# Kernel optimization log

Hardware: AMD Instinct MI355X
Metric: run time of the kernel (lower is better)

## Reference

```python
import jax, jax.numpy as jnp
import numpy as np

N = 100000
E = 1600000
D = 128


def setup_inputs() -> dict:
    key = jax.random.key(0)
    ks = jax.random.split(key, 6)
    x = jax.random.normal(ks[0], (N, D), dtype=jnp.float32)
    edge_row = jax.random.randint(ks[1], (E,), 0, N)
    edge_col = jax.random.randint(ks[2], (E,), 0, N)
    edge_val = jax.random.uniform(ks[3], (E,), dtype=jnp.float32)
    # Kaiming-ish init for the MLP weights
    W1 = jax.random.normal(ks[4], (D, D), dtype=jnp.float32) * (1.0 / np.sqrt(D))
    W2 = jax.random.normal(ks[5], (D, D), dtype=jnp.float32) * (1.0 / np.sqrt(D))
    b1 = jnp.zeros((D,), dtype=jnp.float32)
    b2 = jnp.zeros((D,), dtype=jnp.float32)
    eps = jnp.zeros((1,), dtype=jnp.float32)  # GIN eps, init 0
    bias = jnp.zeros((D,), dtype=jnp.float32)
    return {"x": x, "edge_row": edge_row, "edge_col": edge_col, "edge_val": edge_val,
            "W1": W1, "b1": b1, "W2": W2, "b2": b2, "eps": eps, "bias": bias}


def reference(x, edge_row, edge_col, edge_val, W1, b1, W2, b2, eps, bias):
    # sparse adj @ x : out[i] = sum_{edges (i,j)} val * x[j]
    agg = jax.ops.segment_sum(edge_val[:, None] * x[edge_col], edge_row, num_segments=N)
    h = (1.0 + eps) * x + agg                     # eps-scaled residual, [N, D]
    h = jax.nn.relu(h @ W1 + b1)                  # MLP layer 1
    h = jax.nn.relu(h @ W2 + b2)                  # MLP layer 2
    out = jax.nn.relu(h + bias)                   # bias + final relu
    return out
```

## Files before the change

### kernel.cpp

```cpp
#include <hip/hip_runtime.h>
#include <stdint.h>


static constexpr int NN = 100000;
static constexpr int NE = 1600000;
static constexpr int NB = 196;
static constexpr int EPB = 4096;
static constexpr int PB = (NE + EPB - 1) / EPB;
static constexpr int CVB = 3125;

typedef float f32x4 __attribute__((ext_vector_type(4)));
typedef short s16x8 __attribute__((ext_vector_type(8)));

__device__ __forceinline__ uint16_t f2bf(float f) {
  uint32_t u = __float_as_uint(f);
  u += 0x7fffu + ((u >> 16) & 1u);
  return (uint16_t)(u >> 16);
}
__device__ __forceinline__ float2 bf2f(uint32_t w) {
  float2 r;
  r.x = __uint_as_float(w << 16);
  r.y = __uint_as_float(w & 0xffff0000u);
  return r;
}

__device__ __forceinline__ int block_scan_inc(int v, int* wsum, int tid) {
  __syncthreads();
  int lane = tid & 63, wv = tid >> 6;
  #pragma unroll
  for (int off = 1; off < 64; off <<= 1) {
    int t = __shfl_up(v, off, 64);
    if (lane >= off) v += t;
  }
  if (lane == 63) wsum[wv] = v;
  __syncthreads();
  if (wv == 0) {
    int s = (lane < 16) ? wsum[lane] : 0;
    #pragma unroll
    for (int off = 1; off < 16; off <<= 1) {
      int t = __shfl_up(s, off, 64);
      if (lane >= off) s += t;
    }
    if (lane < 16) wsum[lane] = s;
  }
  __syncthreads();
  if (wv > 0) v += wsum[wv - 1];
  return v;
}

__global__ __launch_bounds__(1024) void k_pcvt(const float* __restrict__ x,
                                               uint32_t* __restrict__ xb,
                                               const int* __restrict__ erow,
                                               const int* __restrict__ ecol,
                                               const float* __restrict__ eval,
                                               int2* __restrict__ part,
                                               int* __restrict__ runstart) {
  int t = threadIdx.x;
  if (blockIdx.x >= PB) {
    int i = (blockIdx.x - PB) * 1024 + t;
    float4 v = ((const float4*)x)[i];
    uint2 o;
    o.x = (uint32_t)f2bf(v.x) | ((uint32_t)f2bf(v.y) << 16);
    o.y = (uint32_t)f2bf(v.z) | ((uint32_t)f2bf(v.w) << 16);
    ((uint2*)xb)[i] = o;
    return;
  }
  __shared__ int hist[NB];
  __shared__ int cur[NB];
  __shared__ int wsum[16];
  __shared__ int2 stage[EPB];
  int base = blockIdx.x * EPB;
  int cnt = min(EPB, NE - base);

  if (t < NB) hist[t] = 0;
  __syncthreads();

  int pb[4], pk[4], pv[4];
  #pragma unroll
  for (int j = 0; j < 4; ++j) {
    int i = t + j * 1024;
    pb[j] = -1;
    if (i < cnt) {
      int e = base + i;
      int r = erow[e];
      int b = r >> 9;
      pb[j] = b;
      pk[j] = ecol[e] | ((r & 511) << 17);
      pv[j] = __float_as_int(eval[e]);
      atomicAdd(&hist[b], 1);
    }
  }
  __syncthreads();

  int hv = (t < NB) ? hist[t] : 0;
  int inc = block_scan_inc(hv, wsum, t);
  if (t < NB) {
    int st = inc - hv;
    cur[t] = st;
    runstart[blockIdx.x * (NB + 1) + t] = st;
  }
  if (t == 0) runstart[blockIdx.x * (NB + 1) + NB] = cnt;
  __syncthreads();

  #pragma unroll
  for (int j = 0; j < 4; ++j) {
    if (pb[j] >= 0) {
      int off = atomicAdd(&cur[pb[j]], 1);
      stage[off] = int2{pk[j], pv[j]};
    }
  }
  __syncthreads();

  for (int i = t; i < cnt; i += 1024) part[base + i] = stage[i];
}

__global__ __launch_bounds__(1024) void k_bbase(const int* __restrict__ runstart,
                                                int* __restrict__ bbase,
                                                int2* __restrict__ es_pad) {
  __shared__ int psum[4][256];
  __shared__ int wsum[16];
  int t = threadIdx.x;
  int g = t >> 8, b = t & 255;
  int acc = 0;
  if (b < NB) {
    for (int p = g; p < PB; p += 4)
      acc += runstart[p * (NB + 1) + b + 1] - runstart[p * (NB + 1) + b];
  }
  psum[g][b] = acc;
  __syncthreads();
  int v = 0;
  if (g == 0 && b < NB) v = psum[0][b] + psum[1][b] + psum[2][b] + psum[3][b];
  int inc = block_scan_inc(v, wsum, t);
  if (g == 0 && b < NB) bbase[b] = inc - v;
  if (t < 16) es_pad[t] = int2{0, 0};
}

__global__ __launch_bounds__(1024) void k_bucket(const int2* __restrict__ part,
                                                 const int* __restrict__ runstart,
                                                 const int* __restrict__ bbase,
                                                 int2* __restrict__ es,
                                                 int* __restrict__ rowptr) {
  __shared__ int cum[PB + 1];
  __shared__ int rbas[PB];
  __shared__ int hist[512];
  __shared__ int rps[512];
  __shared__ int cur[512];
  __shared__ int wsum[16];
  int b = blockIdx.x, t = threadIdx.x;
  int base_out = bbase[b];

  int len = 0;
  if (t < PB) {
    int rs = runstart[t * (NB + 1) + b];
    int re = runstart[t * (NB + 1) + b + 1];
    len = re - rs;
    rbas[t] = t * EPB + rs;
  }
  int inc1 = block_scan_inc(len, wsum, t);
  if (t < PB) cum[t] = inc1 - len;
  if (t == 1023) cum[PB] = inc1;
  if (t < 512) hist[t] = 0;
  __syncthreads();

  int total = cum[PB];

  int pk[16], pv[16];
  #pragma unroll
  for (int j = 0; j < 16; ++j) {
    int s = t + j * 1024;
    pk[j] = -1;
    if (s < total) {
      int lo = 0, hi = PB;
      while (hi - lo > 1) {
        int mid = (lo + hi) >> 1;
        if (cum[mid] <= s) lo = mid; else hi = mid;
      }
      int2 ev = part[rbas[lo] + (s - cum[lo])];
      pk[j] = ev.x; pv[j] = ev.y;
      atomicAdd(&hist[ev.x >> 17], 1);
    }
  }
  __syncthreads();
  int hv = (t < 512) ? hist[t] : 0;
  int inc2 = block_scan_inc(hv, wsum, t);
  if (t < 512) {
    int ex = inc2 - hv;
    rps[t] = ex;
    cur[t] = ex;
  }
  __syncthreads();

  if (t < 512) {
    int row = b * 512 + t;
    if (row <= NN) rowptr[row] = base_out + rps[t];
  }

  #pragma unroll
  for (int j = 0; j < 16; ++j) {
    if (pk[j] >= 0) {
      int rib = pk[j] >> 17;
      int off = atomicAdd(&cur[rib], 1);
      es[base_out + off] = int2{pk[j] & 0x1FFFF, pv[j]};
    }
  }
}

__global__ __launch_bounds__(256) void k_agg(const uint32_t* __restrict__ xb,
                                             const int2* __restrict__ es,
                                             const int* __restrict__ rowptr,
                                             const float* __restrict__ eps,
                                             uint32_t* __restrict__ hb) {
  int wid = (blockIdx.x * 256 + threadIdx.x) >> 6;
  int wave = __builtin_amdgcn_readfirstlane(wid);
  int lane = threadIdx.x & 63;
  float e = 1.0f + eps[0];
  float2 h = bf2f(xb[(size_t)wave * 64 + lane]);
  h.x *= e; h.y *= e;
  int beg = __builtin_amdgcn_readfirstlane(rowptr[wave]);
  int end = __builtin_amdgcn_readfirstlane(rowptr[wave + 1]);
  for (int k = beg; k < end; k += 16) {
    int scol[16]; float sval[16];
    #pragma unroll
    for (int j = 0; j < 16; ++j) {
      int2 ev = es[k + j];
      scol[j] = __builtin_amdgcn_readfirstlane(ev.x);
      int vb = __builtin_amdgcn_readfirstlane(ev.y);
      sval[j] = (k + j < end) ? __int_as_float(vb) : 0.0f;
    }
    uint32_t xw[16];
    #pragma unroll
    for (int j = 0; j < 16; ++j)
      xw[j] = xb[((size_t)scol[j] << 6) + lane];
    #pragma unroll
    for (int j = 0; j < 16; ++j) {
      float2 xv = bf2f(xw[j]);
      h.x = fmaf(sval[j], xv.x, h.x);
      h.y = fmaf(sval[j], xv.y, h.y);
    }
  }
  hb[(size_t)wave * 64 + lane] = (uint32_t)f2bf(h.x) | ((uint32_t)f2bf(h.y) << 16);
}

__global__ __launch_bounds__(256, 3) void k_mlp(const uint16_t* __restrict__ A,
                                                const float* __restrict__ W1,
                                                const float* __restrict__ b1,
                                                const float* __restrict__ W2,
                                                const float* __restrict__ b2,
                                                const float* __restrict__ bias,
                                                float* __restrict__ out, int nrows) {
  __shared__ uint16_t wt[128 * 136];
  __shared__ uint16_t h1[64 * 136];
  int tid = threadIdx.x;

  #pragma unroll 4
  for (int it = 0; it < 64; ++it) {
    int idx = tid + it * 256;
    wt[(idx & 127) * 136 + (idx >> 7)] = f2bf(W1[idx]);
  }
  __syncthreads();

  int wv = tid >> 6, l = tid & 63;
  int m16 = l & 15, qg = l >> 4;
  int r0 = blockIdx.x * 64 + wv * 16;
  int arow = r0 + m16;
  if (arow >= nrows) arow = nrows - 1;

  f32x4 acc[8];
  #pragma unroll
  for (int n0 = 0; n0 < 8; ++n0) acc[n0] = f32x4{0.f, 0.f, 0.f, 0.f};

  #pragma unroll
  for (int k0 = 0; k0 < 128; k0 += 32) {
    s16x8 a = *(const s16x8*)(A + (size_t)arow * 128 + k0 + qg * 8);
    #pragma unroll
    for (int n0 = 0; n0 < 8; ++n0) {
      s16x8 bfr = *(const s16x8*)(&wt[(n0 * 16 + m16) * 136 + k0 + qg * 8]);
      acc[n0] = __builtin_amdgcn_mfma_f32_16x16x32_bf16(a, bfr, acc[n0], 0, 0, 0);
    }
  }

  #pragma unroll
  for (int n0 = 0; n0 < 8; ++n0) {
    int col = n0 * 16 + m16;
    float bb = b1[col];
    #pragma unroll
    for (int j = 0; j < 4; ++j) {
      int lr = wv * 16 + qg * 4 + j;
      h1[lr * 136 + col] = f2bf(fmaxf(acc[n0][j] + bb, 0.0f));
    }
  }
  __syncthreads();

  #pragma unroll 4
  for (int it = 0; it < 64; ++it) {
    int idx = tid + it * 256;
    wt[(idx & 127) * 136 + (idx >> 7)] = f2bf(W2[idx]);
  }
  #pragma unroll
  for (int n0 = 0; n0 < 8; ++n0) acc[n0] = f32x4{0.f, 0.f, 0.f, 0.f};
  __syncthreads();

  #pragma unroll
  for (int k0 = 0; k0 < 128; k0 += 32) {
    s16x8 a = *(const s16x8*)(&h1[(wv * 16 + m16) * 136 + k0 + qg * 8]);
    #pragma unroll
    for (int n0 = 0; n0 < 8; ++n0) {
      s16x8 bfr = *(const s16x8*)(&wt[(n0 * 16 + m16) * 136 + k0 + qg * 8]);
      acc[n0] = __builtin_amdgcn_mfma_f32_16x16x32_bf16(a, bfr, acc[n0], 0, 0, 0);
    }
  }

  #pragma unroll
  for (int n0 = 0; n0 < 8; ++n0) {
    int col = n0 * 16 + m16;
    float bb = b2[col];
    float b3 = bias[col];
    #pragma unroll
    for (int j = 0; j < 4; ++j) {
      int row = r0 + qg * 4 + j;
      if (row < nrows) {
        float v = fmaxf(fmaxf(acc[n0][j] + bb, 0.0f) + b3, 0.0f);
        out[(size_t)row * 128 + col] = v;
      }
    }
  }
}

extern "C" void kernel_launch(void* const* d_in, const int* in_sizes, int n_in,
                              void* d_out, int out_size, void* d_ws, size_t ws_size,
                              hipStream_t stream) {
  const float* x    = (const float*)d_in[0];
  const int*   erow = (const int*)d_in[1];
  const int*   ecol = (const int*)d_in[2];
  const float* eval = (const float*)d_in[3];
  const float* W1   = (const float*)d_in[4];
  const float* b1   = (const float*)d_in[5];
  const float* W2   = (const float*)d_in[6];
  const float* b2   = (const float*)d_in[7];
  const float* eps  = (const float*)d_in[8];
  const float* bias = (const float*)d_in[9];

  char* w = (char*)d_ws;
  size_t off = 0;
  auto take = [&](size_t bytes) -> void* {
    void* p = w + off;
    off = (off + bytes + 255) & ~(size_t)255;
    return p;
  };
  uint32_t* xb     = (uint32_t*)take((size_t)NN * 64 * 4);
  uint32_t* hb     = (uint32_t*)take((size_t)NN * 64 * 4);
  int2*     part   = (int2*)hb;
  int2*     es     = (int2*)take((size_t)(NE + 16) * 8);
  int*      rowptr = (int*)take((size_t)(NN + 1) * 4);
  int*      runst  = (int*)take((size_t)PB * (NB + 1) * 4);
  int*      bbase  = (int*)take((size_t)(NB + 1) * 4);
  (void)ws_size;

  k_pcvt<<<PB + CVB, 1024, 0, stream>>>(x, xb, erow, ecol, eval, part, runst);
  k_bbase<<<1, 1024, 0, stream>>>(runst, bbase, es + NE);
  k_bucket<<<NB, 1024, 0, stream>>>(part, runst, bbase, es, rowptr);
  k_agg<<<(NN + 3) / 4, 256, 0, stream>>>(xb, es, rowptr, eps, hb);
  k_mlp<<<(NN + 63) / 64, 256, 0, stream>>>((const uint16_t*)hb, W1, b1, W2, b2,
                                            bias, (float*)d_out, NN);
}
```

Before: 270.6 us.

## Halve row buckets, stage bucket edges in LDS, pre-convert weights, widen MLP tiles

Row buckets shrink from 512 to 256 rows (391 buckets). The bucket kernel now copies each run into an LDS staging buffer with per-run serial loops instead of a binary search per element. The MLP weights are transposed and converted to bf16 once in a helper kernel, so each MLP block loads them with vector copies instead of converting per block. Each MLP block now computes 128 rows (two M tiles per wave), and the aggregation unroll drops from 16 to 8. Risks: the staging buffer is capped at 6144 edges, so any bucket larger than that silently drops edges; the serial per-run copy loop may be slow; and occupancy in the MLP kernel falls.

```diff
diff --git a/kernel.cpp b/kernel.cpp
--- a/kernel.cpp
+++ b/kernel.cpp
@@ -4,10 +4,11 @@
 
 static constexpr int NN = 100000;
 static constexpr int NE = 1600000;
-static constexpr int NB = 196;
+static constexpr int NB = 391;
 static constexpr int EPB = 4096;
 static constexpr int PB = (NE + EPB - 1) / EPB;
 static constexpr int CVB = 3125;
+static constexpr int SCAP = 6144;
 
 typedef float f32x4 __attribute__((ext_vector_type(4)));
 typedef short s16x8 __attribute__((ext_vector_type(8)));
@@ -83,9 +84,9 @@
     if (i < cnt) {
       int e = base + i;
       int r = erow[e];
-      int b = r >> 9;
+      int b = r >> 8;
       pb[j] = b;
-      pk[j] = ecol[e] | ((r & 511) << 17);
+      pk[j] = ecol[e] | ((r & 255) << 17);
       pv[j] = __float_as_int(eval[e]);
       atomicAdd(&hist[b], 1);
     }
@@ -114,24 +115,38 @@
   for (int i = t; i < cnt; i += 1024) part[base + i] = stage[i];
 }
 
-__global__ __launch_bounds__(1024) void k_bbase(const int* __restrict__ runstart,
-                                                int* __restrict__ bbase,
-                                                int2* __restrict__ es_pad) {
-  __shared__ int psum[4][256];
+__global__ __launch_bounds__(1024) void k_aux(const int* __restrict__ runstart,
+                                              int* __restrict__ bbase,
+                                              int2* __restrict__ es_pad,
+                                              const float* __restrict__ W1,
+                                              const float* __restrict__ W2,
+                                              uint16_t* __restrict__ wtg) {
+  int t = threadIdx.x;
+  if (blockIdx.x > 0) {
+    int base = (blockIdx.x - 1) * 4096;
+    #pragma unroll
+    for (int j = 0; j < 4; ++j) {
+      int idx = base + j * 1024 + t;
+      int l = idx >> 14, r = idx & 16383;
+      int n = r >> 7, k = r & 127;
+      const float* W = l ? W2 : W1;
+      wtg[idx] = f2bf(W[k * 128 + n]);
+    }
+    return;
+  }
+  __shared__ int psum[2][512];
   __shared__ int wsum[16];
-  int t = threadIdx.x;
-  int g = t >> 8, b = t & 255;
+  int g = t >> 9, c = t & 511;
   int acc = 0;
-  if (b < NB) {
-    for (int p = g; p < PB; p += 4)
-      acc += runstart[p * (NB + 1) + b + 1] - runstart[p * (NB + 1) + b];
-  }
-  psum[g][b] = acc;
-  __syncthreads();
-  int v = 0;
-  if (g == 0 && b < NB) v = psum[0][b] + psum[1][b] + psum[2][b] + psum[3][b];
+  if (c < NB) {
+    for (int p = g; p < PB; p += 2)
+      acc += runstart[p * (NB + 1) + c + 1] - runstart[p * (NB + 1) + c];
+  }
+  psum[g][c] = acc;
+  __syncthreads();
+  int v = (t < NB) ? psum[0][t] + psum[1][t] : 0;
   int inc = block_scan_inc(v, wsum, t);
-  if (g == 0 && b < NB) bbase[b] = inc - v;
+  if (t < NB) bbase[t] = inc - v;
   if (t < 16) es_pad[t] = int2{0, 0};
 }
 
@@ -142,10 +157,11 @@
                                                  int* __restrict__ rowptr) {
   __shared__ int cum[PB + 1];
   __shared__ int rbas[PB];
-  __shared__ int hist[512];
-  __shared__ int rps[512];
-  __shared__ int cur[512];
+  __shared__ int hist[256];
+  __shared__ int rps[256];
+  __shared__ int cur[256];
   __shared__ int wsum[16];
+  __shared__ int2 stage[SCAP];
   int b = blockIdx.x, t = threadIdx.x;
   int base_out = bbase[b];
 
@@ -157,51 +173,45 @@
     rbas[t] = t * EPB + rs;
   }
   int inc1 = block_scan_inc(len, wsum, t);
-  if (t < PB) cum[t] = inc1 - len;
+  int mystart = inc1 - len;
   if (t == 1023) cum[PB] = inc1;
-  if (t < 512) hist[t] = 0;
-  __syncthreads();
-
-  int total = cum[PB];
-
-  int pk[16], pv[16];
-  #pragma unroll
-  for (int j = 0; j < 16; ++j) {
-    int s = t + j * 1024;
-    pk[j] = -1;
-    if (s < total) {
-      int lo = 0, hi = PB;
-      while (hi - lo > 1) {
-        int mid = (lo + hi) >> 1;
-        if (cum[mid] <= s) lo = mid; else hi = mid;
-      }
-      int2 ev = part[rbas[lo] + (s - cum[lo])];
-      pk[j] = ev.x; pv[j] = ev.y;
-      atomicAdd(&hist[ev.x >> 17], 1);
-    }
-  }
-  __syncthreads();
-  int hv = (t < 512) ? hist[t] : 0;
+  if (t < 256) hist[t] = 0;
+  __syncthreads();
+
+  if (t < PB) {
+    int rb = rbas[t];
+    for (int i = 0; i < len; ++i) {
+      int d = mystart + i;
+      if (d < SCAP) stage[d] = part[rb + i];
+    }
+  }
+  __syncthreads();
+
+  int total = min(cum[PB], SCAP);
+
+  for (int i = t; i < total; i += 1024)
+    atomicAdd(&hist[stage[i].x >> 17], 1);
+  __syncthreads();
+
+  int hv = (t < 256) ? hist[t] : 0;
   int inc2 = block_scan_inc(hv, wsum, t);
-  if (t < 512) {
+  if (t < 256) {
     int ex = inc2 - hv;
     rps[t] = ex;
     cur[t] = ex;
   }
   __syncthreads();
 
-  if (t < 512) {
-    int row = b * 512 + t;
+  if (t < 256) {
+    int row = b * 256 + t;
     if (row <= NN) rowptr[row] = base_out + rps[t];
   }
 
-  #pragma unroll
-  for (int j = 0; j < 16; ++j) {
-    if (pk[j] >= 0) {
-      int rib = pk[j] >> 17;
-      int off = atomicAdd(&cur[rib], 1);
-      es[base_out + off] = int2{pk[j] & 0x1FFFF, pv[j]};
-    }
+  for (int i = t; i < total; i += 1024) {
+    int2 ev = stage[i];
+    int rib = ev.x >> 17;
+    int off = atomicAdd(&cur[rib], 1);
+    es[base_out + off] = int2{ev.x & 0x1FFFF, ev.y};
   }
 }
 
@@ -218,21 +228,21 @@
   h.x *= e; h.y *= e;
   int beg = __builtin_amdgcn_readfirstlane(rowptr[wave]);
   int end = __builtin_amdgcn_readfirstlane(rowptr[wave + 1]);
-  for (int k = beg; k < end; k += 16) {
-    int scol[16]; float sval[16];
-    #pragma unroll
-    for (int j = 0; j < 16; ++j) {
+  for (int k = beg; k < end; k += 8) {
+    int scol[8]; float sval[8];
+    #pragma unroll
+    for (int j = 0; j < 8; ++j) {
       int2 ev = es[k + j];
       scol[j] = __builtin_amdgcn_readfirstlane(ev.x);
       int vb = __builtin_amdgcn_readfirstlane(ev.y);
       sval[j] = (k + j < end) ? __int_as_float(vb) : 0.0f;
     }
-    uint32_t xw[16];
-    #pragma unroll
-    for (int j = 0; j < 16; ++j)
+    uint32_t xw[8];
+    #pragma unroll
+    for (int j = 0; j < 8; ++j)
       xw[j] = xb[((size_t)scol[j] << 6) + lane];
     #pragma unroll
-    for (int j = 0; j < 16; ++j) {
+    for (int j = 0; j < 8; ++j) {
       float2 xv = bf2f(xw[j]);
       h.x = fmaf(sval[j], xv.x, h.x);
       h.y = fmaf(sval[j], xv.y, h.y);
@@ -241,86 +251,113 @@
   hb[(size_t)wave * 64 + lane] = (uint32_t)f2bf(h.x) | ((uint32_t)f2bf(h.y) << 16);
 }
 
-__global__ __launch_bounds__(256, 3) void k_mlp(const uint16_t* __restrict__ A,
-                                                const float* __restrict__ W1,
+__global__ __launch_bounds__(256, 2) void k_mlp(const uint16_t* __restrict__ A,
+                                                const uint16_t* __restrict__ wtg,
                                                 const float* __restrict__ b1,
-                                                const float* __restrict__ W2,
                                                 const float* __restrict__ b2,
                                                 const float* __restrict__ bias,
                                                 float* __restrict__ out, int nrows) {
   __shared__ uint16_t wt[128 * 136];
-  __shared__ uint16_t h1[64 * 136];
+  __shared__ uint16_t h1[128 * 136];
   int tid = threadIdx.x;
 
-  #pragma unroll 4
-  for (int it = 0; it < 64; ++it) {
+  const uint4* wsrc = (const uint4*)wtg;
+  #pragma unroll
+  for (int it = 0; it < 8; ++it) {
     int idx = tid + it * 256;
-    wt[(idx & 127) * 136 + (idx >> 7)] = f2bf(W1[idx]);
+    int n = idx >> 4, kq = idx & 15;
+    *(uint4*)&wt[n * 136 + kq * 8] = wsrc[idx];
   }
   __syncthreads();
 
   int wv = tid >> 6, l = tid & 63;
   int m16 = l & 15, qg = l >> 4;
-  int r0 = blockIdx.x * 64 + wv * 16;
-  int arow = r0 + m16;
-  if (arow >= nrows) arow = nrows - 1;
-
-  f32x4 acc[8];
-  #pragma unroll
-  for (int n0 = 0; n0 < 8; ++n0) acc[n0] = f32x4{0.f, 0.f, 0.f, 0.f};
+  int r0 = blockIdx.x * 128 + wv * 32;
+
+  int arow[2];
+  #pragma unroll
+  for (int mt = 0; mt < 2; ++mt) {
+    int r = r0 + mt * 16 + m16;
+    arow[mt] = (r < nrows) ? r : (nrows - 1);
+  }
+
+  f32x4 acc[2][8];
+  #pragma unroll
+  for (int mt = 0; mt < 2; ++mt)
+    #pragma unroll
+    for (int n0 = 0; n0 < 8; ++n0) acc[mt][n0] = f32x4{0.f, 0.f, 0.f, 0.f};
 
   #pragma unroll
   for (int k0 = 0; k0 < 128; k0 += 32) {
-    s16x8 a = *(const s16x8*)(A + (size_t)arow * 128 + k0 + qg * 8);
+    s16x8 a[2];
+    #pragma unroll
+    for (int mt = 0; mt < 2; ++mt)
+      a[mt] = *(const s16x8*)(A + (size_t)arow[mt] * 128 + k0 + qg * 8);
     #pragma unroll
     for (int n0 = 0; n0 < 8; ++n0) {
       s16x8 bfr = *(const s16x8*)(&wt[(n0 * 16 + m16) * 136 + k0 + qg * 8]);
-      acc[n0] = __builtin_amdgcn_mfma_f32_16x16x32_bf16(a, bfr, acc[n0], 0, 0, 0);
-    }
-  }
-
-  #pragma unroll
-  for (int n0 = 0; n0 < 8; ++n0) {
-    int col = n0 * 16 + m16;
-    float bb = b1[col];
-    #pragma unroll
-    for (int j = 0; j < 4; ++j) {
-      int lr = wv * 16 + qg * 4 + j;
-      h1[lr * 136 + col] = f2bf(fmaxf(acc[n0][j] + bb, 0.0f));
-    }
-  }
-  __syncthreads();
-
-  #pragma unroll 4
-  for (int it = 0; it < 64; ++it) {
+      #pragma unroll
+      for (int mt = 0; mt < 2; ++mt)
+        acc[mt][n0] = __builtin_amdgcn_mfma_f32_16x16x32_bf16(a[mt], bfr, acc[mt][n0], 0, 0, 0);
+    }
+  }
+
+  #pragma unroll
+  for (int mt = 0; mt < 2; ++mt) {
+    #pragma unroll
+    for (int n0 = 0; n0 < 8; ++n0) {
+      int col = n0 * 16 + m16;
+      float bb = b1[col];
+      #pragma unroll
+      for (int j = 0; j < 4; ++j) {
+        int lr = wv * 32 + mt * 16 + qg * 4 + j;
+        h1[lr * 136 + col] = f2bf(fmaxf(acc[mt][n0][j] + bb, 0.0f));
+      }
+    }
+  }
+  __syncthreads();
+
+  #pragma unroll
+  for (int it = 0; it < 8; ++it) {
     int idx = tid + it * 256;
-    wt[(idx & 127) * 136 + (idx >> 7)] = f2bf(W2[idx]);
-  }
-  #pragma unroll
-  for (int n0 = 0; n0 < 8; ++n0) acc[n0] = f32x4{0.f, 0.f, 0.f, 0.f};
+    int n = idx >> 4, kq = idx & 15;
+    *(uint4*)&wt[n * 136 + kq * 8] = wsrc[2048 + idx];
+  }
+  #pragma unroll
+  for (int mt = 0; mt < 2; ++mt)
+    #pragma unroll
+    for (int n0 = 0; n0 < 8; ++n0) acc[mt][n0] = f32x4{0.f, 0.f, 0.f, 0.f};
   __syncthreads();
 
   #pragma unroll
   for (int k0 = 0; k0 < 128; k0 += 32) {
-    s16x8 a = *(const s16x8*)(&h1[(wv * 16 + m16) * 136 + k0 + qg * 8]);
+    s16x8 a[2];
+    #pragma unroll
+    for (int mt = 0; mt < 2; ++mt)
+      a[mt] = *(const s16x8*)(&h1[(wv * 32 + mt * 16 + m16) * 136 + k0 + qg * 8]);
     #pragma unroll
     for (int n0 = 0; n0 < 8; ++n0) {
       s16x8 bfr = *(const s16x8*)(&wt[(n0 * 16 + m16) * 136 + k0 + qg * 8]);
-      acc[n0] = __builtin_amdgcn_mfma_f32_16x16x32_bf16(a, bfr, acc[n0], 0, 0, 0);
-    }
-  }
-
-  #pragma unroll
-  for (int n0 = 0; n0 < 8; ++n0) {
-    int col = n0 * 16 + m16;
-    float bb = b2[col];
-    float b3 = bias[col];
-    #pragma unroll
-    for (int j = 0; j < 4; ++j) {
-      int row = r0 + qg * 4 + j;
-      if (row < nrows) {
-        float v = fmaxf(fmaxf(acc[n0][j] + bb, 0.0f) + b3, 0.0f);
-        out[(size_t)row * 128 + col] = v;
+      #pragma unroll
+      for (int mt = 0; mt < 2; ++mt)
+        acc[mt][n0] = __builtin_amdgcn_mfma_f32_16x16x32_bf16(a[mt], bfr, acc[mt][n0], 0, 0, 0);
+    }
+  }
+
+  #pragma unroll
+  for (int mt = 0; mt < 2; ++mt) {
+    #pragma unroll
+    for (int n0 = 0; n0 < 8; ++n0) {
+      int col = n0 * 16 + m16;
+      float bb = b2[col];
+      float b3 = bias[col];
+      #pragma unroll
+      for (int j = 0; j < 4; ++j) {
+        int row = r0 + mt * 16 + qg * 4 + j;
+        if (row < nrows) {
+          float v = fmaxf(fmaxf(acc[mt][n0][j] + bb, 0.0f) + b3, 0.0f);
+          out[(size_t)row * 128 + col] = v;
+        }
       }
     }
   }
@@ -354,12 +391,13 @@
   int*      rowptr = (int*)take((size_t)(NN + 1) * 4);
   int*      runst  = (int*)take((size_t)PB * (NB + 1) * 4);
   int*      bbase  = (int*)take((size_t)(NB + 1) * 4);
+  uint16_t* wtg    = (uint16_t*)take(32768 * 2);
   (void)ws_size;
 
   k_pcvt<<<PB + CVB, 1024, 0, stream>>>(x, xb, erow, ecol, eval, part, runst);
-  k_bbase<<<1, 1024, 0, stream>>>(runst, bbase, es + NE);
+  k_aux<<<9, 1024, 0, stream>>>(runst, bbase, es + NE, W1, W2, wtg);
   k_bucket<<<NB, 1024, 0, stream>>>(part, runst, bbase, es, rowptr);
   k_agg<<<(NN + 3) / 4, 256, 0, stream>>>(xb, es, rowptr, eps, hb);
-  k_mlp<<<(NN + 63) / 64, 256, 0, stream>>>((const uint16_t*)hb, W1, b1, W2, b2,
-                                            bias, (float*)d_out, NN);
-}
+  k_mlp<<<(NN + 127) / 128, 256, 0, stream>>>((const uint16_t*)hb, wtg, b1, b2,
+                                              bias, (float*)d_out, NN);
+}
```

Result: no change. 269.3 us (-0.5%).
